# Kernel optimization log

Measured on AMD Instinct MI355X. Metric: run time of the kernel, lower is better.

The kernel has to match this reference:

```python
import jax, jax.numpy as jnp
import numpy as np

# ---- static config (mirrors __init__) ----
OMEGAS = [5.0, 7.0, 9.0, 12.0, 16.0, 22.0, 30.0, 40.0]
XI = 0.05
DT = 0.01
UJ_U1 = 0.01

_decay = (1.0 / (2.0 * np.pi * XI)) * np.log(1.0 / UJ_U1)  # cycles to decay to uj_u1
VALID_W = [int(2.0 * np.pi / w / np.sqrt(1.0 - XI ** 2) * _decay / DT) for w in OMEGAS]
KER = [2 * a - 1 for a in VALID_W]  # per-channel duhamel kernel size (odd)
MAXK = max(KER)
OUT_CH = len(OMEGAS)


def _build_irfs(log_omegas):
    """Analytic impulse-response filter bank, shape [OUT_CH, 1, MAXK]."""
    omegas = jnp.clip(jnp.exp(log_omegas), 0.01, 1000.0)
    sq = jnp.sqrt(jnp.float32(1.0 - XI ** 2))
    rows = []
    for i in range(OUT_CH):  # small fixed loop over channels (distinct static lengths)
        W, K = VALID_W[i], KER[i]
        tt = jnp.arange(W, dtype=jnp.float32) * DT
        omegaD = omegas[i] * sq
        irf = (1.0 / omegaD) * jnp.exp(-XI * omegas[i] * tt) * jnp.sin(omegaD * tt)
        w = jnp.concatenate([irf[::-1], jnp.zeros((K // 2,), jnp.float32)])  # len K
        addpad = MAXK - K  # even, since K and MAXK are both odd
        w = jnp.pad(w, (addpad // 2, addpad // 2))
        rows.append(w)
    return jnp.stack(rows)[:, None, :]  # [O, 1, MAXK]


def setup_inputs() -> dict:
    key = jax.random.key(0)
    x = jax.random.normal(key, (16, 1, 65536), dtype=jnp.float32)
    log_omegas = jnp.log(jnp.asarray(OMEGAS, dtype=jnp.float32))
    return {"inputs": x, "log_omegas": log_omegas}


def reference(inputs, log_omegas):
    irfs = _build_irfs(log_omegas)  # [O,1,MAXK]
    pad = MAXK // 2
    xp = jnp.pad(inputs, ((0, 0), (0, 0), (pad, pad)))
    # torch conv1d is cross-correlation == lax conv (no kernel flip)
    return jax.lax.conv_general_dilated(
        xp, irfs, window_strides=(1,), padding='VALID',
        dimension_numbers=('NCH', 'OIH', 'NCH'))
```

## Files before the change

kernel.cpp:

```cpp
#include <hip/hip_runtime.h>
#include <math.h>


#define N_SAMP  65536
#define NB      16
#define NO      8
#define NT      512
#define LBLK    4096
#define HALO    2048
#define LOOKB   3904
#define TQ      2000

constexpr int CW[NO] = {1844, 1317, 1024, 768, 576, 419, 307, 230};

__device__ __forceinline__ int P(int q) { return q ^ ((q >> 3) & 7); }

__device__ __forceinline__ float rfl(float x) {
    return __int_as_float(__builtin_amdgcn_readfirstlane(__float_as_int(x)));
}

template<int O>
__device__ __forceinline__ void duh_wave(const float* __restrict__ lw,
                                         float* __restrict__ out,
                                         const float* __restrict__ tile,
                                         float* __restrict__ ybuf,
                                         int b, int n0, int t)
{
    constexpr int W   = CW[O];
    constexpr int Wu  = (W + 3) & ~3;
    constexpr int E   = Wu - W;
    constexpr int Q2C = (1856 - Wu) / 4;

    const int lane = t & 63;

    const float omf  = fminf(fmaxf(__expf(lw[O]), 0.01f), 1000.0f);
    const float omD  = omf * 0.99874921777190895f;
    const float th   = omD * 0.01f;
    const float alph = 0.0005f * omf;
    const float r1   = __expf(-alph);
    const float gr = rfl(r1 * __cosf(th)), gi = rfl(r1 * __sinf(th));
    const float rW   = __expf(-alph * (float)W);
    const float aW   = th * (float)W;
    const float binv = 1.0f / omD;
    const float c1   = rfl(binv);
    const float c2   = rfl(binv * rW * __cosf(aW));
    const float cei  = rfl(-binv * rW * __sinf(aW));

    float g2r_ = gr*gr - gi*gi,       g2i_ = 2.f*gr*gi;
    float g3r_ = g2r_*gr - g2i_*gi,   g3i_ = g2r_*gi + g2i_*gr;
    float g4r_ = g2r_*g2r_ - g2i_*g2i_, g4i_ = 2.f*g2r_*g2i_;
    const float G2r = rfl(g2r_), G2i = rfl(g2i_);
    const float G3r = rfl(g3r_), G3i = rfl(g3i_);
    const float G4r = rfl(g4r_), G4i = rfl(g4i_);
    float Mr[7], Mi[7];
    {
        float pr = g4r_*g4r_ - g4i_*g4i_, pq = 2.f*g4r_*g4i_;
        float nr = pr*pr - pq*pq, ni = 2.f*pr*pq; pr = nr; pq = ni;
        nr = pr*pr - pq*pq; ni = 2.f*pr*pq; pr = nr; pq = ni;
#pragma unroll
        for (int k = 0; k < 7; ++k) {
            Mr[k] = rfl(pr); Mi[k] = rfl(pq);
            nr = pr*pr - pq*pq; ni = 2.f*pr*pq; pr = nr; pq = ni;
        }
    }

    float plr = 1.f, pli = 0.f;
#pragma unroll
    for (int k = 0; k < 6; ++k) {
        if ((lane >> k) & 1) {
            const float nr = plr*Mr[k] - pli*Mi[k];
            const float ni = plr*Mi[k] + pli*Mr[k];
            plr = nr; pli = ni;
        }
    }

    float Cr = 0.f, Ci = 0.f;

#define LDQ(q) (*(const float4*)&tile[4 * P(q)])

#pragma unroll
    for (int s = 0; s < 3; ++s) {
        const int q1 = 464 + 512*s + 8*lane;
        const int q2 = Q2C + 512*s + 8*lane;

        float4 lz[8];
        float Br = 0.f, Bi = 0.f;
        float4 d0 = LDQ(q2);
#pragma unroll
        for (int m = 0; m < 8; ++m) {
            const float4 s1 = LDQ(q1 + m);
            const float4 dn = LDQ(q2 + m + 1);
            float e0, e1, e2, e3;
            if constexpr (E == 0)      { e0=d0.x; e1=d0.y; e2=d0.z; e3=d0.w; }
            else if constexpr (E == 1) { e0=d0.y; e1=d0.z; e2=d0.w; e3=dn.x; }
            else if constexpr (E == 2) { e0=d0.z; e1=d0.w; e2=dn.x; e3=dn.y; }
            else                       { e0=d0.w; e1=dn.x; e2=dn.y; e3=dn.z; }
            float4 lq;
#define STEP(xa, xc, slot)                                        \
            {                                                     \
                const float er = fmaf(-c2, (xc), c1 * (xa));      \
                const float ei = cei * (xc);                      \
                const float nr = fmaf(gr, Br, fmaf(-gi, Bi, er)); \
                const float ni = fmaf(gi, Br, fmaf( gr, Bi, ei)); \
                Br = nr; Bi = ni; slot = Bi;                      \
            }
            STEP(s1.x, e0, lq.x); STEP(s1.y, e1, lq.y);
            STEP(s1.z, e2, lq.z); STEP(s1.w, e3, lq.w);
#undef STEP
            lz[m] = lq;
            d0 = dn;
        }

        float Sr = Br, Si = Bi;
#pragma unroll
        for (int k = 0; k < 6; ++k) {
            const int d = 1 << k;
            const float ur = __shfl_up(Sr, d, 64);
            const float ui = __shfl_up(Si, d, 64);
            if (lane >= d) {
                const float nr = fmaf(Mr[k], ur, fmaf(-Mi[k], ui, Sr));
                const float ni = fmaf(Mr[k], ui, fmaf( Mi[k], ur, Si));
                Sr = nr; Si = ni;
            }
        }
        const float Tr = __shfl(Sr, 63, 64);
        const float Ti = __shfl(Si, 63, 64);

        if (s > 0) {
            float exr = __shfl_up(Sr, 1, 64);
            float exi = __shfl_up(Si, 1, 64);
            if (lane == 0) { exr = 0.f; exi = 0.f; }
            const float sr = fmaf(plr, Cr, fmaf(-pli, Ci, exr));
            const float si = fmaf(plr, Ci, fmaf( pli, Cr, exi));
            float wr = fmaf(gr, sr, -(gi * si));
            float wi = fmaf(gi, sr,  (gr * si));
#pragma unroll
            for (int m = 0; m < 8; ++m) {
                float4 y;
                y.x = lz[m].x + wi;
                y.y = fmaf(gi,  wr, fmaf(gr,  wi, lz[m].y));
                y.z = fmaf(G2i, wr, fmaf(G2r, wi, lz[m].z));
                y.w = fmaf(G3i, wr, fmaf(G3r, wi, lz[m].w));
                *(float4*)&ybuf[4 * P(512*O + 8*lane + m)] = y;
                const float nwr = fmaf(G4r, wr, -(G4i * wi));
                const float nwi = fmaf(G4i, wr,  (G4r * wi));
                wr = nwr; wi = nwi;
            }
            __syncthreads();
#pragma unroll
            for (int i = 0; i < 8; ++i) {
                const float4 v = *(const float4*)&ybuf[4 * P(512*i + t)];
                float* op = out + ((size_t)(b*NO + i))*(size_t)N_SAMP
                                + n0 + (s-1)*2048 + 4*t;
                *(float4*)op = v;
            }
            __syncthreads();
        }
        const float nCr = fmaf(Mr[6], Cr, fmaf(-Mi[6], Ci, Tr));
        const float nCi = fmaf(Mr[6], Ci, fmaf( Mi[6], Cr, Ti));
        Cr = rfl(nCr); Ci = rfl(nCi);
    }
#undef LDQ
}

__global__ __launch_bounds__(NT, 2)
void duh_kernel(const float* __restrict__ x, const float* __restrict__ lw,
                float* __restrict__ out)
{
    __shared__ float tile[TQ * 4];
    __shared__ float ybuf[16384];
    const int c  = blockIdx.x;
    const int b  = blockIdx.y;
    const int n0 = c * LBLK;
    const int t  = threadIdx.x;

    const float* xb = x + (size_t)b * N_SAMP;
    const int tstart = n0 - LOOKB;
#pragma unroll
    for (int i = 0; i < 4; ++i) {
        const int k = t + 512 * i;
        if (k < TQ) {
            const int g0 = tstart + 4 * k;
            float4 v;
            if (g0 >= 0) v = *(const float4*)(xb + g0);
            else { v.x = 0.f; v.y = 0.f; v.z = 0.f; v.w = 0.f; }
            *(float4*)&tile[4 * P(k)] = v;
        }
    }
    __syncthreads();

    switch (t >> 6) {
      case 0: duh_wave<0>(lw, out, tile, ybuf, b, n0, t); break;
      case 1: duh_wave<1>(lw, out, tile, ybuf, b, n0, t); break;
      case 2: duh_wave<2>(lw, out, tile, ybuf, b, n0, t); break;
      case 3: duh_wave<3>(lw, out, tile, ybuf, b, n0, t); break;
      case 4: duh_wave<4>(lw, out, tile, ybuf, b, n0, t); break;
      case 5: duh_wave<5>(lw, out, tile, ybuf, b, n0, t); break;
      case 6: duh_wave<6>(lw, out, tile, ybuf, b, n0, t); break;
      default:duh_wave<7>(lw, out, tile, ybuf, b, n0, t); break;
    }
}

extern "C" void kernel_launch(void* const* d_in, const int* in_sizes, int n_in,
                              void* d_out, int out_size, void* d_ws, size_t ws_size,
                              hipStream_t stream) {
    const float* x  = (const float*)d_in[0];
    const float* lw = (const float*)d_in[1];
    float* out = (float*)d_out;

    dim3 grid(N_SAMP / LBLK, NB);
    duh_kernel<<<grid, dim3(NT), 0, stream>>>(x, lw, out);
}
```

Baseline: 18.89 us.

## Shrink warm-up scan to per-channel chunk size and drop block-wide barriers

The lookback warm-up pass, which used to be a full 2048-sample stage per channel, now covers only a per-channel halo length (HS*64 samples) sized to that channel's decay. This cuts the recurrence work and LDS reads spent before the first output. Each wave also gets a private ybuf slice and stores only its own channel's output, so the block-wide __syncthreads around the transpose go away. Twiddle powers are computed directly via exp/cos/sin, which may change numerical accuracy. The reduced halo could truncate the decay tail for low-frequency channels.

```diff
diff --git a/kernel.cpp b/kernel.cpp
--- a/kernel.cpp
+++ b/kernel.cpp
@@ -7,11 +7,11 @@
 #define NO      8
 #define NT      512
 #define LBLK    4096
-#define HALO    2048
 #define LOOKB   3904
 #define TQ      2000
 
-constexpr int CW[NO] = {1844, 1317, 1024, 768, 576, 419, 307, 230};
+constexpr int CW[NO]  = {1844, 1317, 1024, 768, 576, 419, 307, 230};
+constexpr int CHS[NO] = {32, 24, 20, 16, 12, 8, 8, 4};
 
 __device__ __forceinline__ int P(int q) { return q ^ ((q >> 3) & 7); }
 
@@ -23,15 +23,15 @@
 __device__ __forceinline__ void duh_wave(const float* __restrict__ lw,
                                          float* __restrict__ out,
                                          const float* __restrict__ tile,
-                                         float* __restrict__ ybuf,
-                                         int b, int n0, int t)
+                                         float* __restrict__ yw,
+                                         int b, int n0, int lane)
 {
-    constexpr int W   = CW[O];
-    constexpr int Wu  = (W + 3) & ~3;
-    constexpr int E   = Wu - W;
-    constexpr int Q2C = (1856 - Wu) / 4;
-
-    const int lane = t & 63;
+    constexpr int W  = CW[O];
+    constexpr int Wu = (W + 3) & ~3;
+    constexpr int E  = Wu - W;
+    constexpr int QW = Wu / 4;
+    constexpr int HS = CHS[O];
+    constexpr int HQ = HS / 4;
 
     const float omf  = fminf(fmaxf(__expf(lw[O]), 0.01f), 1000.0f);
     const float omD  = omf * 0.99874921777190895f;
@@ -46,71 +46,77 @@
     const float c2   = rfl(binv * rW * __cosf(aW));
     const float cei  = rfl(-binv * rW * __sinf(aW));
 
-    float g2r_ = gr*gr - gi*gi,       g2i_ = 2.f*gr*gi;
-    float g3r_ = g2r_*gr - g2i_*gi,   g3i_ = g2r_*gi + g2i_*gr;
+    float g2r_ = gr*gr - gi*gi,         g2i_ = 2.f*gr*gi;
+    float g3r_ = g2r_*gr - g2i_*gi,     g3i_ = g2r_*gi + g2i_*gr;
     float g4r_ = g2r_*g2r_ - g2i_*g2i_, g4i_ = 2.f*g2r_*g2i_;
     const float G2r = rfl(g2r_), G2i = rfl(g2i_);
     const float G3r = rfl(g3r_), G3i = rfl(g3i_);
     const float G4r = rfl(g4r_), G4i = rfl(g4i_);
-    float Mr[7], Mi[7];
+
+    float Mor[7], Moi[7];
     {
-        float pr = g4r_*g4r_ - g4i_*g4i_, pq = 2.f*g4r_*g4i_;
-        float nr = pr*pr - pq*pq, ni = 2.f*pr*pq; pr = nr; pq = ni;
-        nr = pr*pr - pq*pq; ni = 2.f*pr*pq; pr = nr; pq = ni;
+        const float rl = __expf(-alph * 32.f);
+        const float al = th * 32.f;
+        float pr = rl * __cosf(al), pq = rl * __sinf(al);
 #pragma unroll
         for (int k = 0; k < 7; ++k) {
-            Mr[k] = rfl(pr); Mi[k] = rfl(pq);
-            nr = pr*pr - pq*pq; ni = 2.f*pr*pq; pr = nr; pq = ni;
-        }
-    }
-
+            Mor[k] = rfl(pr); Moi[k] = rfl(pq);
+            const float nr = pr*pr - pq*pq, ni = 2.f*pr*pq;
+            pr = nr; pq = ni;
+        }
+    }
+    float Mhr[6], Mhi[6];
+    {
+        const float rl = __expf(-alph * (float)HS);
+        const float al = th * (float)HS;
+        float pr = rl * __cosf(al), pq = rl * __sinf(al);
+#pragma unroll
+        for (int k = 0; k < 6; ++k) {
+            Mhr[k] = rfl(pr); Mhi[k] = rfl(pq);
+            const float nr = pr*pr - pq*pq, ni = 2.f*pr*pq;
+            pr = nr; pq = ni;
+        }
+    }
     float plr = 1.f, pli = 0.f;
 #pragma unroll
     for (int k = 0; k < 6; ++k) {
         if ((lane >> k) & 1) {
-            const float nr = plr*Mr[k] - pli*Mi[k];
-            const float ni = plr*Mi[k] + pli*Mr[k];
+            const float nr = plr*Mor[k] - pli*Moi[k];
+            const float ni = plr*Moi[k] + pli*Mor[k];
             plr = nr; pli = ni;
         }
     }
 
-    float Cr = 0.f, Ci = 0.f;
-
 #define LDQ(q) (*(const float4*)&tile[4 * P(q)])
-
-#pragma unroll
-    for (int s = 0; s < 3; ++s) {
-        const int q1 = 464 + 512*s + 8*lane;
-        const int q2 = Q2C + 512*s + 8*lane;
-
-        float4 lz[8];
+#define DSEL(e0,e1,e2,e3,d0,dn)                                              \
+    if constexpr (E == 0)      { e0=d0.x; e1=d0.y; e2=d0.z; e3=d0.w; }       \
+    else if constexpr (E == 1) { e0=d0.y; e1=d0.z; e2=d0.w; e3=dn.x; }       \
+    else if constexpr (E == 2) { e0=d0.z; e1=d0.w; e2=dn.x; e3=dn.y; }       \
+    else                       { e0=d0.w; e1=dn.x; e2=dn.y; e3=dn.z; }
+#define STEP(xa, xc)                                              \
+    {                                                             \
+        const float er = fmaf(-c2, (xc), c1 * (xa));              \
+        const float ei = cei * (xc);                              \
+        const float nr = fmaf(gr, Br, fmaf(-gi, Bi, er));         \
+        const float ni = fmaf(gi, Br, fmaf( gr, Bi, ei));         \
+        Br = nr; Bi = ni;                                         \
+    }
+
+    float Cr, Ci;
+    {
         float Br = 0.f, Bi = 0.f;
+        const int q1 = 976 - 16 * HS + HQ * lane;
+        const int q2 = q1 - QW;
         float4 d0 = LDQ(q2);
 #pragma unroll
-        for (int m = 0; m < 8; ++m) {
+        for (int m = 0; m < HQ; ++m) {
             const float4 s1 = LDQ(q1 + m);
             const float4 dn = LDQ(q2 + m + 1);
             float e0, e1, e2, e3;
-            if constexpr (E == 0)      { e0=d0.x; e1=d0.y; e2=d0.z; e3=d0.w; }
-            else if constexpr (E == 1) { e0=d0.y; e1=d0.z; e2=d0.w; e3=dn.x; }
-            else if constexpr (E == 2) { e0=d0.z; e1=d0.w; e2=dn.x; e3=dn.y; }
-            else                       { e0=d0.w; e1=dn.x; e2=dn.y; e3=dn.z; }
-            float4 lq;
-#define STEP(xa, xc, slot)                                        \
-            {                                                     \
-                const float er = fmaf(-c2, (xc), c1 * (xa));      \
-                const float ei = cei * (xc);                      \
-                const float nr = fmaf(gr, Br, fmaf(-gi, Bi, er)); \
-                const float ni = fmaf(gi, Br, fmaf( gr, Bi, ei)); \
-                Br = nr; Bi = ni; slot = Bi;                      \
-            }
-            STEP(s1.x, e0, lq.x); STEP(s1.y, e1, lq.y);
-            STEP(s1.z, e2, lq.z); STEP(s1.w, e3, lq.w);
-#undef STEP
-            lz[m] = lq;
+            DSEL(e0, e1, e2, e3, d0, dn);
+            STEP(s1.x, e0); STEP(s1.y, e1); STEP(s1.z, e2); STEP(s1.w, e3);
             d0 = dn;
         }
-
         float Sr = Br, Si = Bi;
 #pragma unroll
         for (int k = 0; k < 6; ++k) {
@@ -118,48 +124,88 @@
             const float ur = __shfl_up(Sr, d, 64);
             const float ui = __shfl_up(Si, d, 64);
             if (lane >= d) {
-                const float nr = fmaf(Mr[k], ur, fmaf(-Mi[k], ui, Sr));
-                const float ni = fmaf(Mr[k], ui, fmaf( Mi[k], ur, Si));
+                const float nr = fmaf(Mhr[k], ur, fmaf(-Mhi[k], ui, Sr));
+                const float ni = fmaf(Mhr[k], ui, fmaf( Mhi[k], ur, Si));
                 Sr = nr; Si = ni;
             }
         }
+        Cr = rfl(__shfl(Sr, 63, 64));
+        Ci = rfl(__shfl(Si, 63, 64));
+    }
+
+#pragma unroll
+    for (int s = 0; s < 2; ++s) {
+        const int q1 = 976 + 512 * s + 8 * lane;
+        const int q2 = q1 - QW;
+
+        float4 lz[8];
+        float Br = 0.f, Bi = 0.f;
+        float4 d0 = LDQ(q2);
+#pragma unroll
+        for (int m = 0; m < 8; ++m) {
+            const float4 s1 = LDQ(q1 + m);
+            const float4 dn = LDQ(q2 + m + 1);
+            float e0, e1, e2, e3;
+            DSEL(e0, e1, e2, e3, d0, dn);
+            float4 lq;
+            STEP(s1.x, e0); lq.x = Bi;
+            STEP(s1.y, e1); lq.y = Bi;
+            STEP(s1.z, e2); lq.z = Bi;
+            STEP(s1.w, e3); lq.w = Bi;
+            lz[m] = lq;
+            d0 = dn;
+        }
+
+        float Sr = Br, Si = Bi;
+#pragma unroll
+        for (int k = 0; k < 6; ++k) {
+            const int d = 1 << k;
+            const float ur = __shfl_up(Sr, d, 64);
+            const float ui = __shfl_up(Si, d, 64);
+            if (lane >= d) {
+                const float nr = fmaf(Mor[k], ur, fmaf(-Moi[k], ui, Sr));
+                const float ni = fmaf(Mor[k], ui, fmaf( Moi[k], ur, Si));
+                Sr = nr; Si = ni;
+            }
+        }
         const float Tr = __shfl(Sr, 63, 64);
         const float Ti = __shfl(Si, 63, 64);
-
-        if (s > 0) {
-            float exr = __shfl_up(Sr, 1, 64);
-            float exi = __shfl_up(Si, 1, 64);
-            if (lane == 0) { exr = 0.f; exi = 0.f; }
-            const float sr = fmaf(plr, Cr, fmaf(-pli, Ci, exr));
-            const float si = fmaf(plr, Ci, fmaf( pli, Cr, exi));
-            float wr = fmaf(gr, sr, -(gi * si));
-            float wi = fmaf(gi, sr,  (gr * si));
-#pragma unroll
-            for (int m = 0; m < 8; ++m) {
-                float4 y;
-                y.x = lz[m].x + wi;
-                y.y = fmaf(gi,  wr, fmaf(gr,  wi, lz[m].y));
-                y.z = fmaf(G2i, wr, fmaf(G2r, wi, lz[m].z));
-                y.w = fmaf(G3i, wr, fmaf(G3r, wi, lz[m].w));
-                *(float4*)&ybuf[4 * P(512*O + 8*lane + m)] = y;
-                const float nwr = fmaf(G4r, wr, -(G4i * wi));
-                const float nwi = fmaf(G4i, wr,  (G4r * wi));
-                wr = nwr; wi = nwi;
-            }
-            __syncthreads();
-#pragma unroll
-            for (int i = 0; i < 8; ++i) {
-                const float4 v = *(const float4*)&ybuf[4 * P(512*i + t)];
-                float* op = out + ((size_t)(b*NO + i))*(size_t)N_SAMP
-                                + n0 + (s-1)*2048 + 4*t;
-                *(float4*)op = v;
-            }
-            __syncthreads();
-        }
-        const float nCr = fmaf(Mr[6], Cr, fmaf(-Mi[6], Ci, Tr));
-        const float nCi = fmaf(Mr[6], Ci, fmaf( Mi[6], Cr, Ti));
+        float exr = __shfl_up(Sr, 1, 64);
+        float exi = __shfl_up(Si, 1, 64);
+        if (lane == 0) { exr = 0.f; exi = 0.f; }
+
+        const float sr = fmaf(plr, Cr, fmaf(-pli, Ci, exr));
+        const float si = fmaf(plr, Ci, fmaf( pli, Cr, exi));
+
+        float wr = fmaf(gr, sr, -(gi * si));
+        float wi = fmaf(gi, sr,  (gr * si));
+#pragma unroll
+        for (int m = 0; m < 8; ++m) {
+            float4 y;
+            y.x = lz[m].x + wi;
+            y.y = fmaf(gi,  wr, fmaf(gr,  wi, lz[m].y));
+            y.z = fmaf(G2i, wr, fmaf(G2r, wi, lz[m].z));
+            y.w = fmaf(G3i, wr, fmaf(G3r, wi, lz[m].w));
+            *(float4*)&yw[4 * P(8 * lane + m)] = y;
+            const float nwr = fmaf(G4r, wr, -(G4i * wi));
+            const float nwi = fmaf(G4i, wr,  (G4r * wi));
+            wr = nwr; wi = nwi;
+        }
+        float* op = out + ((size_t)(b * NO + O)) * (size_t)N_SAMP
+                        + n0 + s * 2048;
+#pragma unroll
+        for (int i = 0; i < 8; ++i) {
+            const int q = 64 * i + lane;
+            const float4 v = *(const float4*)&yw[4 * P(q)];
+            *(float4*)(op + 4 * q) = v;
+        }
+
+        const float nCr = fmaf(Mor[6], Cr, fmaf(-Moi[6], Ci, Tr));
+        const float nCi = fmaf(Mor[6], Ci, fmaf( Moi[6], Cr, Ti));
         Cr = rfl(nCr); Ci = rfl(nCi);
     }
+#undef STEP
+#undef DSEL
 #undef LDQ
 }
 
@@ -168,7 +214,7 @@
                 float* __restrict__ out)
 {
     __shared__ float tile[TQ * 4];
-    __shared__ float ybuf[16384];
+    __shared__ float ybuf[NO * 2048];
     const int c  = blockIdx.x;
     const int b  = blockIdx.y;
     const int n0 = c * LBLK;
@@ -189,15 +235,18 @@
     }
     __syncthreads();
 
-    switch (t >> 6) {
-      case 0: duh_wave<0>(lw, out, tile, ybuf, b, n0, t); break;
-      case 1: duh_wave<1>(lw, out, tile, ybuf, b, n0, t); break;
-      case 2: duh_wave<2>(lw, out, tile, ybuf, b, n0, t); break;
-      case 3: duh_wave<3>(lw, out, tile, ybuf, b, n0, t); break;
-      case 4: duh_wave<4>(lw, out, tile, ybuf, b, n0, t); break;
-      case 5: duh_wave<5>(lw, out, tile, ybuf, b, n0, t); break;
-      case 6: duh_wave<6>(lw, out, tile, ybuf, b, n0, t); break;
-      default:duh_wave<7>(lw, out, tile, ybuf, b, n0, t); break;
+    const int wv   = t >> 6;
+    const int lane = t & 63;
+    float* yw = ybuf + wv * 2048;
+    switch (wv) {
+      case 0: duh_wave<0>(lw, out, tile, yw, b, n0, lane); break;
+      case 1: duh_wave<1>(lw, out, tile, yw, b, n0, lane); break;
+      case 2: duh_wave<2>(lw, out, tile, yw, b, n0, lane); break;
+      case 3: duh_wave<3>(lw, out, tile, yw, b, n0, lane); break;
+      case 4: duh_wave<4>(lw, out, tile, yw, b, n0, lane); break;
+      case 5: duh_wave<5>(lw, out, tile, yw, b, n0, lane); break;
+      case 6: duh_wave<6>(lw, out, tile, yw, b, n0, lane); break;
+      default:duh_wave<7>(lw, out, tile, yw, b, n0, lane); break;
     }
 }
 
```

Result: faster. 16.69 us (median of 3 runs) (-11.6%).
